# Performance work log

Hardware: AMD Instinct MI355X
Metric: run time of the kernel (lower is better)

## Reference

```python
import jax, jax.numpy as jnp
import numpy as np

B, S, H, N, D = 2, 2048, 1024, 16, 64  # batch, seq, hidden, heads, head_size
PAD = -30000.0


def setup_inputs() -> dict:
    key = jax.random.key(0)
    kx, kqkv, kout, krpe = jax.random.split(key, 4)
    x = jax.random.normal(kx, (B, S, H), jnp.float32)
    qkv = jax.random.normal(kqkv, (H, 3, N, D), jnp.float32) * H ** (-0.5)
    out_w = jax.random.normal(kout, (N, D, H), jnp.float32) * (N * D) ** (-0.5)
    # rpe_bias is zero-init in torch; use small randn so the bias path is exercised
    rpe_bias = jax.random.normal(krpe, (N, S), jnp.float32) * 0.02
    return {"x": x, "qkv": qkv, "out_w": out_w, "rpe_bias": rpe_bias}


def reference(x, qkv, out_w, rpe_bias):
    # q, k, v: [B, N, S, D]
    q, k, v = jnp.einsum('bsx,xMnd->Mbnsd', x, qkv)
    s = x.shape[1]
    a = jnp.einsum('bnsd,bntd->bnst', q, k) * q.shape[-1] ** (-0.5)
    # cumulative relative-position bias: bias[n, i, j] = cumsum(rpe)[n, i-j] for i>=j,
    # PAD otherwise (exactly what to_tril produces on the row-broadcast cumsum).
    cum = jnp.cumsum(rpe_bias[:, :s], axis=-1)            # [N, S]
    rel = jnp.arange(s)[:, None] - jnp.arange(s)[None, :]  # [S, S], i - j
    bias = jnp.where(rel >= 0, cum[:, jnp.clip(rel, 0)], PAD)  # [N, S, S]
    a = jax.nn.softmax(a + bias, axis=-1)
    mix = jnp.einsum('bnst,bntd->bnsd', a, v)
    return jnp.einsum('bnsd,ndx->bsx', mix, out_w)
```

## Files before the change

kernel.cpp:

```cpp
#include <hip/hip_runtime.h>
#include <hip/hip_bf16.h>
#include <cstdint>
#include <cstddef>

#define B_   2
#define S_   2048
#define H_   1024
#define NH   16
#define DH   64
#define LOG2E 1.4426950408889634f
#define SCALE2 (0.125f * LOG2E)

typedef __hip_bfloat16 bf16;
typedef short bf16x8 __attribute__((ext_vector_type(8)));
typedef float f32x4 __attribute__((ext_vector_type(4)));

#define MFMA16(a, b, c) __builtin_amdgcn_mfma_f32_16x16x32_bf16((a), (b), (c), 0, 0, 0)

__device__ __forceinline__ void async16(const void* g, void* l) {
  __builtin_amdgcn_global_load_lds(
      (const __attribute__((address_space(1))) void*)g,
      (__attribute__((address_space(3))) void*)l,
      16, 0, 0);
}
__device__ __forceinline__ void async4(const void* g, void* l) {
  __builtin_amdgcn_global_load_lds(
      (const __attribute__((address_space(1))) void*)g,
      (__attribute__((address_space(3))) void*)l,
      4, 0, 0);
}

__device__ __forceinline__ void tr_body(const float* __restrict__ src,
                                        bf16* __restrict__ dst, int R, int C,
                                        int c0, int r0, bf16 (*tile)[33], int tid) {
  int tx = tid & 31, ty = tid >> 5;
  for (int i = 0; i < 32; i += 8)
    tile[ty + i][tx] = __float2bfloat16(src[(size_t)(r0 + ty + i) * C + c0 + tx]);
  __syncthreads();
  for (int i = 0; i < 32; i += 8)
    dst[(size_t)(c0 + ty + i) * R + r0 + tx] = tile[tx][ty + i];
}

__global__ __launch_bounds__(256)
void prep(const float* __restrict__ x, bf16* __restrict__ xb,
          const float* __restrict__ qkv, bf16* __restrict__ qkvT,
          const float* __restrict__ outw, bf16* __restrict__ outwT,
          const float* __restrict__ rpe, float* __restrict__ cum) {
  __shared__ char pm[2176] __attribute__((aligned(16)));
  const int L = blockIdx.x, tid = threadIdx.x;
  if (L < 4096) {
    int i = (L * 256 + tid) * 4;
    float4 v = *(const float4*)(x + i);
    bf16 o[4] = {__float2bfloat16(v.x), __float2bfloat16(v.y),
                 __float2bfloat16(v.z), __float2bfloat16(v.w)};
    *(uint64_t*)(xb + i) = *(const uint64_t*)o;
  } else if (L < 7168) {
    int t = L - 4096;
    int cx = t % 96, ry = t / 96;
    tr_body(qkv, qkvT, 1024, 3072, cx * 32, ry * 32, (bf16(*)[33])pm, tid);
  } else if (L < 8192) {
    int t = L - 7168;
    int cx = t & 31, ry = t >> 5;
    tr_body(outw, outwT, 1024, 1024, cx * 32, ry * 32, (bf16(*)[33])pm, tid);
  } else {
    float* ssum = (float*)pm;
    int n = L - 8192;
    float loc[8];
    float s = 0.f;
    int base = tid * 8;
#pragma unroll
    for (int u = 0; u < 8; ++u) {
      loc[u] = rpe[n * S_ + base + u];
      s += loc[u];
    }
    ssum[tid] = s;
    __syncthreads();
    float own = s;
    for (int off = 1; off < 256; off <<= 1) {
      float v = (tid >= off) ? ssum[tid - off] : 0.f;
      __syncthreads();
      ssum[tid] += v;
      __syncthreads();
    }
    float run = ssum[tid] - own;
#pragma unroll
    for (int u = 0; u < 8; ++u) {
      run += loc[u];
      cum[n * S_ + base + u] = run * LOG2E;
    }
  }
}

template <int MODE>
__global__ __launch_bounds__(256, MODE == 0 ? 3 : 2)
void gemm_bt(const bf16* __restrict__ A, const bf16* __restrict__ Bt,
             bf16* __restrict__ C0, bf16* __restrict__ C1, bf16* __restrict__ C2,
             float* __restrict__ F0) {
  constexpr int NT = (MODE == 0) ? 4 : 2;
  constexpr int NB = NT * 32;
  __shared__ char smem[MODE == 0 ? 36864 : 12288] __attribute__((aligned(16)));
  bf16* As = (bf16*)smem;
  bf16* Bs = (bf16*)(smem + 8192);
  const int tid = threadIdx.x, lane = tid & 63, w = tid >> 6;
  const int lr = lane & 15, lq = lane >> 4;
  const int m0 = blockIdx.y * 128, n0 = blockIdx.x * NB;
  const int wm = (w & 1) * 64, wn = (w >> 1) * (NT * 16);

  f32x4 acc[4][NT] = {};

  for (int k0 = 0; k0 < 1024; k0 += 32) {
    __syncthreads();
#pragma unroll
    for (int t = 0; t < 2; ++t) {
      int c = (t * 4 + w) * 64 + lane;
      int row = c >> 2, ch = c & 3;
      int k8 = (ch ^ ((row >> 1) & 3)) * 8;
      async16(A + (size_t)(m0 + row) * 1024 + k0 + k8,
              (char*)As + (size_t)(t * 4 + w) * 1024 + lane * 16);
    }
#pragma unroll
    for (int t = 0; t < NB / 64; ++t) {
      int c = (t * 4 + w) * 64 + lane;
      int row = c >> 2, ch = c & 3;
      int k8 = (ch ^ ((row >> 1) & 3)) * 8;
      async16(Bt + (size_t)(n0 + row) * 1024 + k0 + k8,
              (char*)Bs + (size_t)(t * 4 + w) * 1024 + lane * 16);
    }
    __syncthreads();
    bf16x8 af[4], bfr[NT];
#pragma unroll
    for (int mt = 0; mt < 4; ++mt) {
      int row = wm + mt * 16 + lr;
      af[mt] = *(const bf16x8*)(As + row * 32 + ((lq ^ ((row >> 1) & 3)) << 3));
    }
#pragma unroll
    for (int nt = 0; nt < NT; ++nt) {
      int row = wn + nt * 16 + lr;
      bfr[nt] = *(const bf16x8*)(Bs + row * 32 + ((lq ^ ((row >> 1) & 3)) << 3));
    }
#pragma unroll
    for (int mt = 0; mt < 4; ++mt)
#pragma unroll
      for (int nt = 0; nt < NT; ++nt)
        acc[mt][nt] = MFMA16(af[mt], bfr[nt], acc[mt][nt]);
  }

  if (MODE == 0) {
    __syncthreads();
    bf16* E = (bf16*)smem + w * (64 * 72);
    const int cbase = n0 + wn;
    const int mm = cbase >> 10, nn = (cbase >> 6) & 15;
    const int bb = (m0 + wm) >> 11;
    const int sbase = (m0 + wm) & 2047;
    if (mm < 2) {
#pragma unroll
      for (int mt = 0; mt < 4; ++mt)
#pragma unroll
        for (int nt = 0; nt < 4; ++nt)
#pragma unroll
          for (int r = 0; r < 4; ++r)
            E[(mt * 16 + lq * 4 + r) * 72 + nt * 16 + lr] =
                __float2bfloat16(acc[mt][nt][r]);
      bf16* dst = (mm == 0 ? C0 : C1) +
                  ((size_t)(bb * NH + nn) * S_ + sbase) * DH;
#pragma unroll
      for (int it = 0; it < 8; ++it) {
        int c = it * 64 + lane;
        int rw = c >> 3, c8 = c & 7;
        *(uint4*)(dst + (size_t)rw * DH + c8 * 8) =
            *(const uint4*)(E + rw * 72 + c8 * 8);
      }
    } else {
#pragma unroll
      for (int mt = 0; mt < 4; ++mt)
#pragma unroll
        for (int nt = 0; nt < 4; ++nt)
#pragma unroll
          for (int r = 0; r < 4; ++r)
            E[(nt * 16 + lr) * 72 + mt * 16 + lq * 4 + r] =
                __float2bfloat16(acc[mt][nt][r]);
      bf16* dst = C2 + (size_t)(bb * NH + nn) * DH * S_;
#pragma unroll
      for (int it = 0; it < 8; ++it) {
        int c = it * 64 + lane;
        int dr = c >> 3, c8 = c & 7;
        *(uint4*)(dst + (size_t)dr * S_ + sbase + c8 * 8) =
            *(const uint4*)(E + dr * 72 + c8 * 8);
      }
    }
  } else {
#pragma unroll
    for (int mt = 0; mt < 4; ++mt)
#pragma unroll
      for (int nt = 0; nt < NT; ++nt)
#pragma unroll
        for (int r = 0; r < 4; ++r) {
          int rM = m0 + wm + mt * 16 + lq * 4 + r;
          int cN = n0 + wn + nt * 16 + lr;
          F0[(size_t)rM * 1024 + cN] = acc[mt][nt][r];
        }
  }
}

__device__ __forceinline__ void fa_stage(const bf16* __restrict__ k,
                                         const bf16* __restrict__ vt,
                                         const float* __restrict__ cumn,
                                         char* smem, int bn, int i0, int j0,
                                         int buf, int tid) {
  char* dst = smem + buf * 16384;
  const char* ksrc = (const char*)(k + ((size_t)bn * S_ + j0) * DH);
#pragma unroll
  for (int t = 0; t < 2; ++t) {
    int c = t * 256 + tid;
    int row = c >> 3, ch = c & 7;
    int cs = ch ^ (row & 7);
    async16(ksrc + row * 128 + cs * 16, dst + c * 16);
  }
  const char* vsrc = (const char*)(vt + (size_t)bn * DH * S_);
#pragma unroll
  for (int t = 0; t < 2; ++t) {
    int c = t * 256 + tid;
    int row = c >> 3, ch = c & 7;
    int cs = ch ^ (row & 7);
    async16(vsrc + (size_t)row * (S_ * 2) + j0 * 2 + cs * 16,
            dst + 8192 + c * 16);
  }
  if (tid < 136) {
    float* cdst = (float*)(smem + 41984) + buf * 544;
    int base = i0 - j0 - 63 + tid;
#pragma unroll
    for (int p = 0; p < 4; ++p) {
      int src = base + p;
      src = src < 0 ? 0 : (src > S_ - 1 ? S_ - 1 : src);
      async4(cumn + src, cdst + p * 136 + tid);
    }
  }
}

__global__ __launch_bounds__(256, 2)
void fa_kernel(const bf16* __restrict__ q, const bf16* __restrict__ k,
               const bf16* __restrict__ vt, const float* __restrict__ cum,
               bf16* __restrict__ mix) {
  __shared__ char smem[46592] __attribute__((aligned(16)));
  bf16* Ps = (bf16*)(smem + 32768);
  float* combL = (float*)(smem + 46336);

  const int tid = threadIdx.x, lane = tid & 63, w = tid >> 6;
  const int lr = lane & 15, lq = lane >> 4;
  const int rg = w & 1, jh = w >> 1;

  const int L = blockIdx.x;
  const int xcd = L & 7, slot = L >> 3;
  const int bn = xcd + 8 * (slot & 3);
  const int pp = slot >> 2;
  const int n = bn & (NH - 1);
  const int b = bn >> 4;
  const float* cumn = cum + n * S_;

  const int T0 = 31 - pp;
  const int T1 = pp;
  const int nu0 = T0 + 1;

  bf16x8 ones;
#pragma unroll
  for (int u = 0; u < 8; ++u) ones[u] = (short)0x3F80;
  const f32x4 fz = {0.f, 0.f, 0.f, 0.f};

  bf16x8 qf[2][2];
  f32x4 oacc[2][4];
  f32x4 lacc[2];

  fa_stage(k, vt, cumn, smem, bn, T0 * 64, 0, 0, tid);

  int ti = T0, jt = 0, i0 = T0 * 64;

  for (int g = 0; g < 33; ++g) {
    const int bsel = g & 1;
    const char* kb = smem + bsel * 16384;
    const char* vb = kb + 8192;
    const float* cumB = (const float*)(smem + 41984) + bsel * 544;
    const int j0 = jt * 64;
    const bool diag = (jt == ti);

    __syncthreads();

    if (g + 1 < 33) {
      int gn = g + 1, tin, jtn;
      if (gn < nu0) { tin = T0; jtn = gn; }
      else          { tin = T1; jtn = gn - nu0; }
      fa_stage(k, vt, cumn, smem, bn, tin * 64, jtn * 64, bsel ^ 1, tid);
    }

    if (jt == 0) {
      const bf16* qbase = q + ((size_t)bn * S_ + i0 + rg * 32) * DH;
#pragma unroll
      for (int is = 0; is < 2; ++is) {
#pragma unroll
        for (int kt = 0; kt < 2; ++kt)
          qf[is][kt] = *(const bf16x8*)(qbase + (is * 16 + lr) * DH + kt * 32 + lq * 8);
        lacc[is] = fz;
#pragma unroll
        for (int dt = 0; dt < 4; ++dt) oacc[is][dt] = fz;
      }
    }

    f32x4 sa[2][2] = {};
#pragma unroll
    for (int kt = 0; kt < 2; ++kt)
#pragma unroll
      for (int nt = 0; nt < 2; ++nt) {
        int krow = jh * 32 + nt * 16 + lr;
        bf16x8 kf = *(const bf16x8*)(kb + krow * 128 +
                        (((kt * 4 + lq) ^ (krow & 7)) << 4));
        sa[0][nt] = MFMA16(kf, qf[0][kt], sa[0][nt]);
        sa[1][nt] = MFMA16(kf, qf[1][kt], sa[1][nt]);
      }

    const int doff = i0 - j0;
#pragma unroll
    for (int is = 0; is < 2; ++is) {
      const int ilocI = rg * 32 + is * 16 + lr;
      if (!diag) {
#pragma unroll
        for (int nt = 0; nt < 2; ++nt) {
          int jl = jh * 32 + nt * 16 + lq * 4;
          int Xm3 = 60 + ilocI - jl;
          int ph = Xm3 & 3, b0 = Xm3 & ~3;
          f32x4 cv = *(const f32x4*)(cumB + ph * 136 + b0);
          bf16 pk[4];
#pragma unroll
          for (int r = 0; r < 4; ++r)
            pk[r] = __float2bfloat16(exp2f(sa[is][nt][r] * SCALE2 + cv[3 - r]));
          *(uint64_t*)(Ps + ilocI * 72 + jl) = *(const uint64_t*)pk;
        }
      } else {
#pragma unroll
        for (int nt = 0; nt < 2; ++nt) {
          int jl = jh * 32 + nt * 16 + lq * 4;
          int Xm3 = 60 + ilocI - jl;
          int ph = Xm3 & 3, b0 = Xm3 & ~3;
          f32x4 cv = *(const f32x4*)(cumB + ph * 136 + b0);
          bf16 pk[4];
#pragma unroll
          for (int r = 0; r < 4; ++r) {
            float pv = (doff + ilocI - jl - r >= 0)
                           ? exp2f(sa[is][nt][r] * SCALE2 + cv[3 - r])
                           : 0.f;
            pk[r] = __float2bfloat16(pv);
          }
          *(uint64_t*)(Ps + ilocI * 72 + jl) = *(const uint64_t*)pk;
        }
      }
    }

    {
      bf16x8 pf0 = *(const bf16x8*)(Ps + (rg * 32 + lr) * 72 + jh * 32 + lq * 8);
      bf16x8 pf1 = *(const bf16x8*)(Ps + (rg * 32 + 16 + lr) * 72 + jh * 32 + lq * 8);
      lacc[0] = MFMA16(pf0, ones, lacc[0]);
      lacc[1] = MFMA16(pf1, ones, lacc[1]);
#pragma unroll
      for (int dt = 0; dt < 4; ++dt) {
        int vrow = dt * 16 + lr;
        bf16x8 vf = *(const bf16x8*)(vb + vrow * 128 +
                        (((jh * 4 + lq) ^ (vrow & 7)) << 4));
        oacc[0][dt] = MFMA16(pf0, vf, oacc[0][dt]);
        oacc[1][dt] = MFMA16(pf1, vf, oacc[1][dt]);
      }
    }

    if (diag) {
      __syncthreads();
      float* scr = (float*)(smem + bsel * 16384) + rg * 2048;
      if (jh == 1) {
#pragma unroll
        for (int is = 0; is < 2; ++is) {
#pragma unroll
          for (int dt = 0; dt < 4; ++dt)
#pragma unroll
            for (int r = 0; r < 4; ++r) {
              int row = is * 16 + lq * 4 + r;
              int col = ((dt ^ lq) << 4) + lr;
              scr[row * 64 + col] = oacc[is][dt][r];
            }
          if (lr == 0)
#pragma unroll
            for (int r = 0; r < 4; ++r)
              combL[rg * 32 + is * 16 + lq * 4 + r] = lacc[is][r];
        }
      }
      __syncthreads();
      if (jh == 0) {
#pragma unroll
        for (int is = 0; is < 2; ++is) {
#pragma unroll
          for (int r = 0; r < 4; ++r)
            lacc[is][r] += combL[rg * 32 + is * 16 + lq * 4 + r];
#pragma unroll
          for (int dt = 0; dt < 4; ++dt)
#pragma unroll
            for (int r = 0; r < 4; ++r) {
              int row = is * 16 + lq * 4 + r;
              int col = ((dt ^ lq) << 4) + lr;
              oacc[is][dt][r] += scr[row * 64 + col];
            }
        }
#pragma unroll
        for (int is = 0; is < 2; ++is)
#pragma unroll
          for (int dt = 0; dt < 4; ++dt)
#pragma unroll
            for (int r = 0; r < 4; ++r) {
              int i = i0 + rg * 32 + is * 16 + lq * 4 + r;
              int d = dt * 16 + lr;
              mix[((size_t)(b * S_ + i) * NH + n) * DH + d] =
                  __float2bfloat16(oacc[is][dt][r] / lacc[is][r]);
            }
      }
      ti = T1; jt = 0; i0 = T1 * 64;
    } else {
      ++jt;
    }
  }
}

extern "C" void kernel_launch(void* const* d_in, const int* in_sizes, int n_in,
                              void* d_out, int out_size, void* d_ws, size_t ws_size,
                              hipStream_t stream) {
  const float* x     = (const float*)d_in[0];
  const float* qkv   = (const float*)d_in[1];
  const float* out_w = (const float*)d_in[2];
  const float* rpe   = (const float*)d_in[3];
  float* out = (float*)d_out;

  char* ws = (char*)d_ws;
  bf16* qkvT  = (bf16*)(ws + 0);
  bf16* outwT = (bf16*)(ws + 6291456);
  bf16* xb    = (bf16*)(ws + 8388608);
  bf16* qb    = (bf16*)(ws + 16777216);
  bf16* kb    = (bf16*)(ws + 25165824);
  bf16* vtb   = (bf16*)(ws + 33554432);
  bf16* mixb  = (bf16*)(ws + 41943040);
  float* cum  = (float*)(ws + 50331648);

  prep<<<8208, 256, 0, stream>>>(x, xb, qkv, qkvT, out_w, outwT, rpe, cum);
  gemm_bt<0><<<dim3(3072 / 128, 4096 / 128), 256, 0, stream>>>(xb, qkvT, qb, kb, vtb, nullptr);
  fa_kernel<<<512, 256, 0, stream>>>(qb, kb, vtb, cum, mixb);
  gemm_bt<1><<<dim3(1024 / 64, 4096 / 128), 256, 0, stream>>>(mixb, outwT, nullptr, nullptr, nullptr, out);
}
```

Before: 184.8 us.

## Keep softmax probabilities in registers by permuting K rows to match MFMA operand layout

Reorders which K rows each lane loads for the QK^T MFMA (with a matching LDS swizzle) so the score accumulator layout lines up with the A-operand layout of the PV MFMA. The exponentiated probabilities can then be packed straight into bf16x8 registers, with no round trip through a shared-memory P tile. This removes the P stores, the reloads and the LDS footprint of that buffer, which shrinks shared memory per block. The cost is a non-trivial index remapping that must stay consistent with the swizzle and with the causal and bias offsets.

```diff
diff --git a/kernel.cpp b/kernel.cpp
--- a/kernel.cpp
+++ b/kernel.cpp
@@ -28,6 +28,11 @@
       (const __attribute__((address_space(1))) void*)g,
       (__attribute__((address_space(3))) void*)l,
       4, 0, 0);
+}
+
+__device__ __forceinline__ short bf16bits(float v) {
+  bf16 t = __float2bfloat16(v);
+  return *reinterpret_cast<short*>(&t);
 }
 
 __device__ __forceinline__ void tr_body(const float* __restrict__ src,
@@ -213,7 +218,7 @@
   for (int t = 0; t < 2; ++t) {
     int c = t * 256 + tid;
     int row = c >> 3, ch = c & 7;
-    int cs = ch ^ (row & 7);
+    int cs = ch ^ ((row & 3) | ((row >> 1) & 4));
     async16(ksrc + row * 128 + cs * 16, dst + c * 16);
   }
   const char* vsrc = (const char*)(vt + (size_t)bn * DH * S_);
@@ -226,7 +231,7 @@
             dst + 8192 + c * 16);
   }
   if (tid < 136) {
-    float* cdst = (float*)(smem + 41984) + buf * 544;
+    float* cdst = (float*)(smem + 32768) + buf * 544;
     int base = i0 - j0 - 63 + tid;
 #pragma unroll
     for (int p = 0; p < 4; ++p) {
@@ -241,9 +246,8 @@
 void fa_kernel(const bf16* __restrict__ q, const bf16* __restrict__ k,
                const bf16* __restrict__ vt, const float* __restrict__ cum,
                bf16* __restrict__ mix) {
-  __shared__ char smem[46592] __attribute__((aligned(16)));
-  bf16* Ps = (bf16*)(smem + 32768);
-  float* combL = (float*)(smem + 46336);
+  __shared__ char smem[37376] __attribute__((aligned(16)));
+  float* combL = (float*)(smem + 37120);
 
   const int tid = threadIdx.x, lane = tid & 63, w = tid >> 6;
   const int lr = lane & 15, lq = lane >> 4;
@@ -266,6 +270,8 @@
   for (int u = 0; u < 8; ++u) ones[u] = (short)0x3F80;
   const f32x4 fz = {0.f, 0.f, 0.f, 0.f};
 
+  const int kkey = (lr & 3) | (((lr >> 2) & 1) << 2);
+
   bf16x8 qf[2][2];
   f32x4 oacc[2][4];
   f32x4 lacc[2];
@@ -278,7 +284,7 @@
     const int bsel = g & 1;
     const char* kb = smem + bsel * 16384;
     const char* vb = kb + 8192;
-    const float* cumB = (const float*)(smem + 41984) + bsel * 544;
+    const float* cumB = (const float*)(smem + 32768) + bsel * 544;
     const int j0 = jt * 64;
     const bool diag = (jt == ti);
 
@@ -309,63 +315,50 @@
     for (int kt = 0; kt < 2; ++kt)
 #pragma unroll
       for (int nt = 0; nt < 2; ++nt) {
-        int krow = jh * 32 + nt * 16 + lr;
+        int krow = jh * 32 + ((lr >> 2) << 3) + nt * 4 + (lr & 3);
         bf16x8 kf = *(const bf16x8*)(kb + krow * 128 +
-                        (((kt * 4 + lq) ^ (krow & 7)) << 4));
+                        (((kt * 4 + lq) ^ kkey) << 4));
         sa[0][nt] = MFMA16(kf, qf[0][kt], sa[0][nt]);
         sa[1][nt] = MFMA16(kf, qf[1][kt], sa[1][nt]);
       }
 
     const int doff = i0 - j0;
+    bf16x8 pf[2];
 #pragma unroll
     for (int is = 0; is < 2; ++is) {
       const int ilocI = rg * 32 + is * 16 + lr;
-      if (!diag) {
-#pragma unroll
-        for (int nt = 0; nt < 2; ++nt) {
-          int jl = jh * 32 + nt * 16 + lq * 4;
-          int Xm3 = 60 + ilocI - jl;
-          int ph = Xm3 & 3, b0 = Xm3 & ~3;
-          f32x4 cv = *(const f32x4*)(cumB + ph * 136 + b0);
-          bf16 pk[4];
+#pragma unroll
+      for (int nt = 0; nt < 2; ++nt) {
+        int jl = jh * 32 + lq * 8 + nt * 4;
+        int Xm3 = 60 + ilocI - jl;
+        int ph = Xm3 & 3, b0 = Xm3 & ~3;
+        f32x4 cv = *(const f32x4*)(cumB + ph * 136 + b0);
+        if (!diag) {
 #pragma unroll
           for (int r = 0; r < 4; ++r)
-            pk[r] = __float2bfloat16(exp2f(sa[is][nt][r] * SCALE2 + cv[3 - r]));
-          *(uint64_t*)(Ps + ilocI * 72 + jl) = *(const uint64_t*)pk;
-        }
-      } else {
-#pragma unroll
-        for (int nt = 0; nt < 2; ++nt) {
-          int jl = jh * 32 + nt * 16 + lq * 4;
-          int Xm3 = 60 + ilocI - jl;
-          int ph = Xm3 & 3, b0 = Xm3 & ~3;
-          f32x4 cv = *(const f32x4*)(cumB + ph * 136 + b0);
-          bf16 pk[4];
+            pf[is][nt * 4 + r] =
+                bf16bits(exp2f(sa[is][nt][r] * SCALE2 + cv[3 - r]));
+        } else {
 #pragma unroll
           for (int r = 0; r < 4; ++r) {
             float pv = (doff + ilocI - jl - r >= 0)
                            ? exp2f(sa[is][nt][r] * SCALE2 + cv[3 - r])
                            : 0.f;
-            pk[r] = __float2bfloat16(pv);
+            pf[is][nt * 4 + r] = bf16bits(pv);
           }
-          *(uint64_t*)(Ps + ilocI * 72 + jl) = *(const uint64_t*)pk;
         }
       }
     }
 
-    {
-      bf16x8 pf0 = *(const bf16x8*)(Ps + (rg * 32 + lr) * 72 + jh * 32 + lq * 8);
-      bf16x8 pf1 = *(const bf16x8*)(Ps + (rg * 32 + 16 + lr) * 72 + jh * 32 + lq * 8);
-      lacc[0] = MFMA16(pf0, ones, lacc[0]);
-      lacc[1] = MFMA16(pf1, ones, lacc[1]);
-#pragma unroll
-      for (int dt = 0; dt < 4; ++dt) {
-        int vrow = dt * 16 + lr;
-        bf16x8 vf = *(const bf16x8*)(vb + vrow * 128 +
-                        (((jh * 4 + lq) ^ (vrow & 7)) << 4));
-        oacc[0][dt] = MFMA16(pf0, vf, oacc[0][dt]);
-        oacc[1][dt] = MFMA16(pf1, vf, oacc[1][dt]);
-      }
+    lacc[0] = MFMA16(pf[0], ones, lacc[0]);
+    lacc[1] = MFMA16(pf[1], ones, lacc[1]);
+#pragma unroll
+    for (int dt = 0; dt < 4; ++dt) {
+      int vrow = dt * 16 + lr;
+      bf16x8 vf = *(const bf16x8*)(vb + vrow * 128 +
+                      (((jh * 4 + lq) ^ (vrow & 7)) << 4));
+      oacc[0][dt] = MFMA16(pf[0], vf, oacc[0][dt]);
+      oacc[1][dt] = MFMA16(pf[1], vf, oacc[1][dt]);
     }
 
     if (diag) {
```

Result: no change. 182.4 us (-1.3%).
